# Performance work log

Measured on AMD Instinct MI355X. Metric: run time of the kernel, lower is better.

Reference implementation:

```python
import jax, jax.numpy as jnp
import numpy as np

B, L, DIN, DT, NOUT = 2, 144, 1024, 150, 4


def setup_inputs() -> dict:
    key = jax.random.key(0)
    ks = jax.random.split(key, 7)
    w = lambda k, shape: (jax.random.normal(k, shape, jnp.float32) * 0.02)
    return dict(
        x=jax.random.normal(ks[0], (B, L, DIN), jnp.float32),
        W_sh=w(ks[1], (DIN, DT)), b_sh=jnp.zeros((DT,), jnp.float32),
        W_st=w(ks[2], (DIN, DT)), b_st=jnp.zeros((DT,), jnp.float32),
        W_oh=w(ks[3], (DIN, DT)), b_oh=jnp.zeros((DT,), jnp.float32),
        W_ot=w(ks[4], (DIN, DT)), b_ot=jnp.zeros((DT,), jnp.float32),
        W_tri1=w(ks[5], (NOUT, DT, DT, DT)),
        W_tri2=w(ks[6], (NOUT, DT, DT, DT)),
    )


def _triaffine(x, y, z, W):
    # supar Triaffine convention: out[b,z,x,y,o] = sum_{i,k,j} x[b,x,i] W[o,i,k,j] y[b,y,j] z[b,z,k]
    w = jnp.einsum('bzk,oikj->bzoij', z, W)      # [B,L,o,d,d]
    t = jnp.einsum('bzoij,byj->bzoiy', w, y)     # [B,L,o,d,L]
    return jnp.einsum('bzoiy,bxi->bzxyo', t, x)  # [B,L,L,L,o]


def reference(x, W_sh, b_sh, W_st, b_st, W_oh, b_oh, W_ot, b_ot, W_tri1, W_tri2):
    # MLP projections (dropout is identity at eval time)
    sh = x @ W_sh + b_sh
    st = x @ W_st + b_st
    oh = x @ W_oh + b_oh
    ot = x @ W_ot + b_ot
    n = x.shape[1]
    # torch .triu() on (..., sh, st) keeps entries with sh <= st, zeros the rest
    tri = jnp.arange(n)[:, None] <= jnp.arange(n)[None, :]
    m = tri[None, :, :, None, None]
    # shstoh = Triaffine(st, rel_oh, sh) -> [b, sh, st, oh, o]; triu over (sh, st)
    s1 = _triaffine(st, oh, sh, W_tri1)
    s1 = jnp.where(m, s1, 0.0)
    # shstot = Triaffine(rel_ot, st, sh) -> [b, sh, ot, st, o]; permutes give (b, sh, st, ot, o) with triu over (sh, st)
    s2 = _triaffine(ot, st, sh, W_tri2)
    s2 = jnp.where(m, jnp.transpose(s2, (0, 1, 3, 2, 4)), 0.0)
    return jax.nn.log_softmax(s1, axis=-1), jax.nn.log_softmax(s2, axis=-1)
```

## Files before the change

### kernel.cpp

```cpp
#include <hip/hip_runtime.h>
#include <hip/hip_bf16.h>
#include <math.h>

typedef unsigned short u16;
typedef __attribute__((ext_vector_type(8))) short bf16x8;
typedef __attribute__((ext_vector_type(8))) unsigned short us8;
typedef __attribute__((ext_vector_type(4))) float f32x4;

static __device__ __forceinline__ u16 f2bf(float f) {
  __hip_bfloat16 h = __float2bfloat16(f);
  return *reinterpret_cast<u16*>(&h);
}

__global__ __launch_bounds__(256) void conv_x(const float* __restrict__ x,
                                              u16* __restrict__ xb) {
  int idx = (blockIdx.x * 256 + threadIdx.x) * 4;
  float4 v = *(const float4*)(x + idx);
  ushort4 o;
  o.x = f2bf(v.x); o.y = f2bf(v.y); o.z = f2bf(v.z); o.w = f2bf(v.w);
  *(ushort4*)(xb + idx) = o;
}

__global__ __launch_bounds__(256) void trans_wp(
    const float* __restrict__ W0, const float* __restrict__ W1,
    const float* __restrict__ W2, const float* __restrict__ W3,
    u16* __restrict__ WT4) {
  __shared__ float lds[64 * 151];
  int kt = blockIdx.x, p = blockIdx.y;
  const float* W = (p == 0) ? W0 : (p == 1) ? W1 : (p == 2) ? W2 : W3;
  for (int t = threadIdx.x; t < 64 * 150; t += 256) {
    int k = t / 150, j = t - k * 150;
    lds[k * 151 + j] = W[(size_t)(kt * 64 + k) * 150 + j];
  }
  __syncthreads();
  u16* dst = WT4 + (size_t)p * 160 * 1024 + kt * 64;
  for (int t = threadIdx.x; t < 160 * 64; t += 256) {
    int j = t >> 6, kk = t & 63;
    float v = (j < 150) ? lds[kk * 151 + j] : 0.f;
    dst[(size_t)j * 1024 + kk] = f2bf(v);
  }
}

__global__ __launch_bounds__(256) void transw_kernel(
    const float* __restrict__ W, u16* __restrict__ WtT) {
  __shared__ float lds[150 * 82];
  int oi = blockIdx.x, jh = blockIdx.y;
  const float* src = W + (size_t)oi * 22500 + jh * 80;
  for (int t = threadIdx.x; t < 150 * 40; t += 256) {
    int k = t / 40, c = t - k * 40;
    if (jh * 80 + 2 * c < 150) {
      float2 v = *(const float2*)(src + (size_t)k * 150 + 2 * c);
      *(float2*)&lds[k * 82 + 2 * c] = v;
    }
  }
  __syncthreads();
  u16* dst = WtT + (size_t)oi * 25600 + (size_t)jh * 80 * 160;
  for (int t = threadIdx.x; t < 80 * 20; t += 256) {
    int jl = t / 20, kc = t - jl * 20;
    int j = jh * 80 + jl;
    bool jlive = (j < 150);
    us8 v;
#pragma unroll
    for (int u = 0; u < 8; ++u) {
      int k = kc * 8 + u;
      float f = (jlive && k < 150) ? lds[k * 82 + jl] : 0.f;
      v[u] = f2bf(f);
    }
    *(us8*)(dst + (size_t)jl * 160 + kc * 8) = v;
  }
}

template <int STAGE>
__global__ __launch_bounds__(192) void gemm_ds(
    const u16* __restrict__ A, const u16* __restrict__ B, u16* __restrict__ C,
    int Mvalid, int ZcapW, int ZcapT, const float* __restrict__ bias0,
    const float* __restrict__ bias1, const float* __restrict__ bias2,
    const float* __restrict__ bias3) {
  constexpr int KS = (STAGE == 0) ? 32 : 5;
  constexpr int AS = (STAGE == 0) ? 1024 : 160;
  const u16 *Ab, *Bb;
  u16* Cb = nullptr;
  int cstride = 0;
  int mrow0 = 0;
  if (STAGE == 0) {
    mrow0 = blockIdx.y * 144;
    Ab = A + (size_t)mrow0 * 1024;
    Bb = B + (size_t)blockIdx.x * 80 * 1024;
  } else if (STAGE == 1) {
    int ntile = blockIdx.x, oi = blockIdx.y, b = blockIdx.z;
    int o = oi / 150, i = oi - o * 150;
    Ab = A + (size_t)b * 23040;
    Bb = B + (size_t)oi * 25600 + ntile * 12800;
    Cb = C + (size_t)b * ZcapW + ((size_t)o * 160 + i) * 160 + ntile * 80;
    cstride = 102400;
  } else {
    int ntile = blockIdx.x, f2 = blockIdx.y, b = blockIdx.z;
    Ab = A + (size_t)b * 23040;
    Bb = B + (size_t)b * ZcapW + (size_t)f2 * 25600 + ntile * 12800;
    Cb = C + (size_t)b * ZcapT + (size_t)f2 * 23040 + ntile * 80;
    cstride = 160;
  }
  int tid = threadIdx.x;
  int lane = tid & 63, wave = tid >> 6;
  int l16 = lane & 15, quad = lane >> 4;
  const u16* Ap = Ab + (size_t)(wave * 48 + l16) * AS + quad * 8;
  const u16* Bp = Bb + (size_t)l16 * AS + quad * 8;
  f32x4 acc[3][5];
#pragma unroll
  for (int mi = 0; mi < 3; ++mi)
#pragma unroll
    for (int ni = 0; ni < 5; ++ni) acc[mi][ni] = (f32x4){0.f, 0.f, 0.f, 0.f};

#pragma unroll
  for (int ks = 0; ks < KS; ++ks) {
    bf16x8 af[3], bfr[5];
#pragma unroll
    for (int mi = 0; mi < 3; ++mi)
      af[mi] = *(const bf16x8*)(Ap + (size_t)mi * 16 * AS + ks * 32);
#pragma unroll
    for (int ni = 0; ni < 5; ++ni)
      bfr[ni] = *(const bf16x8*)(Bp + (size_t)ni * 16 * AS + ks * 32);
#pragma unroll
    for (int mi = 0; mi < 3; ++mi)
#pragma unroll
      for (int ni = 0; ni < 5; ++ni)
        acc[mi][ni] = __builtin_amdgcn_mfma_f32_16x16x32_bf16(
            af[mi], bfr[ni], acc[mi][ni], 0, 0, 0);
  }

  if (STAGE == 0) {
    int nbase = blockIdx.x * 80;
#pragma unroll
    for (int ni = 0; ni < 5; ++ni) {
      int n = nbase + ni * 16 + l16;
      int p = n / 160, j = n - p * 160;
      const float* bp =
          (p == 0) ? bias0 : (p == 1) ? bias1 : (p == 2) ? bias2 : bias3;
      bool live = (j < 150);
      float bv = live ? bp[j] : 0.f;
#pragma unroll
      for (int mi = 0; mi < 3; ++mi) {
        int row = mrow0 + wave * 48 + mi * 16 + quad * 4;
#pragma unroll
        for (int r = 0; r < 4; ++r) {
          float v = live ? acc[mi][ni][r] + bv : 0.f;
          C[((size_t)p * 288 + row + r) * 160 + j] = f2bf(v);
        }
      }
    }
  } else {
#pragma unroll
    for (int mi = 0; mi < 3; ++mi) {
      int grow0 = wave * 48 + mi * 16 + quad * 4;
#pragma unroll
      for (int ni = 0; ni < 5; ++ni)
#pragma unroll
        for (int r = 0; r < 4; ++r) {
          int grow = grow0 + r;
          if (grow < Mvalid)
            Cb[(size_t)grow * cstride + ni * 16 + l16] = f2bf(acc[mi][ni][r]);
        }
    }
  }
}

template <int VAR>
__global__ __launch_bounds__(256) void stage3_kernel(
    const u16* __restrict__ tb, const u16* __restrict__ P,
    float* __restrict__ out, int z0, int ZcapT) {
  __shared__ float sf[9216];
  int bx = blockIdx.x;
  int b = bx & 1, xt = (bx >> 1) * 48;
  int yt = blockIdx.y * 48;
  int zl = blockIdx.z;
  int zg = z0 + zl;
  int tid = threadIdx.x;
  const float NL4 = -1.3862943611198906f;
  size_t obase = ((size_t)(b * 144 + zg)) * 82944;
  if (zg > xt + 47) {
    float4 v = make_float4(NL4, NL4, NL4, NL4);
    for (int p = tid; p < 2304; p += 256) {
      int xl = p / 48, yl = p - xl * 48;
      *(float4*)(out + obase + ((size_t)(xt + xl) * 144 + yt + yl) * 4) = v;
    }
    return;
  }
  int pbase = (VAR == 0) ? xt : yt;
  int qbase = (VAR == 0) ? yt : xt;
  int lane = tid & 63, o = tid >> 6, l16 = lane & 15, quad = lane >> 4;
  const u16* Pp = P + (size_t)b * 23040 + (size_t)(pbase + l16) * 160 + quad * 8;
  const u16* Tp = tb + (size_t)b * ZcapT + (size_t)zl * 92160 +
                  (size_t)(o * 144 + qbase + l16) * 160 + quad * 8;
  const u16* Ap = (VAR == 0) ? Pp : Tp;
  const u16* Bp = (VAR == 0) ? Tp : Pp;
  f32x4 acc[3][3];
#pragma unroll
  for (int mi = 0; mi < 3; ++mi)
#pragma unroll
    for (int ni = 0; ni < 3; ++ni) acc[mi][ni] = (f32x4){0.f, 0.f, 0.f, 0.f};

#pragma unroll
  for (int ks = 0; ks < 5; ++ks) {
    bf16x8 af[3], bfr[3];
#pragma unroll
    for (int mi = 0; mi < 3; ++mi)
      af[mi] = *(const bf16x8*)(Ap + (size_t)mi * 16 * 160 + ks * 32);
#pragma unroll
    for (int ni = 0; ni < 3; ++ni)
      bfr[ni] = *(const bf16x8*)(Bp + (size_t)ni * 16 * 160 + ks * 32);
#pragma unroll
    for (int mi = 0; mi < 3; ++mi)
#pragma unroll
      for (int ni = 0; ni < 3; ++ni)
        acc[mi][ni] = __builtin_amdgcn_mfma_f32_16x16x32_bf16(
            af[mi], bfr[ni], acc[mi][ni], 0, 0, 0);
  }

#pragma unroll
  for (int mi = 0; mi < 3; ++mi)
#pragma unroll
    for (int ni = 0; ni < 3; ++ni)
#pragma unroll
      for (int r = 0; r < 4; ++r)
        sf[((mi * 16 + quad * 4 + r) * 48 + ni * 16 + l16) * 4 + o] =
            acc[mi][ni][r];
  __syncthreads();
  for (int p = tid; p < 2304; p += 256) {
    int xl = p / 48, yl = p - xl * 48;
    int xg = xt + xl;
    float4 v;
    if (zg > xg) {
      v = make_float4(NL4, NL4, NL4, NL4);
    } else {
      float c0 = sf[p * 4], c1 = sf[p * 4 + 1];
      float c2 = sf[p * 4 + 2], c3 = sf[p * 4 + 3];
      float mx = fmaxf(fmaxf(c0, c1), fmaxf(c2, c3));
      float l = mx + logf(expf(c0 - mx) + expf(c1 - mx) + expf(c2 - mx) +
                          expf(c3 - mx));
      v = make_float4(c0 - l, c1 - l, c2 - l, c3 - l);
    }
    *(float4*)(out + obase + ((size_t)xg * 144 + yt + yl) * 4) = v;
  }
}

extern "C" void kernel_launch(void* const* d_in, const int* in_sizes, int n_in,
                              void* d_out, int out_size, void* d_ws,
                              size_t ws_size, hipStream_t stream) {
  const float* x = (const float*)d_in[0];
  const float* Wsh = (const float*)d_in[1];
  const float* bsh = (const float*)d_in[2];
  const float* Wst = (const float*)d_in[3];
  const float* bst = (const float*)d_in[4];
  const float* Woh = (const float*)d_in[5];
  const float* boh = (const float*)d_in[6];
  const float* Wot = (const float*)d_in[7];
  const float* bot = (const float*)d_in[8];
  const float* Wt1 = (const float*)d_in[9];
  const float* Wt2 = (const float*)d_in[10];

  u16* ws = (u16*)d_ws;
  u16* xb = ws;
  u16* WT4 = ws + 294912;
  u16* pAll = ws + 950272;
  u16* WtT = ws + 1134592;
  u16* dyn = ws + 16494592;
  size_t ws_u = ws_size / 2;
  long long avail = (long long)ws_u - 16494592LL;
  int Zc = (avail > 0) ? (int)(avail / 389120) : 1;
  if (Zc > 144) Zc = 144;
  if (Zc < 1) Zc = 1;
  int ZcapW = Zc * 102400, ZcapT = Zc * 92160;
  u16* wbuf = dyn;
  u16* tbuf = dyn + (size_t)2 * ZcapW;

  conv_x<<<288, 256, 0, stream>>>(x, xb);
  trans_wp<<<dim3(16, 4), 256, 0, stream>>>(Wsh, Wst, Woh, Wot, WT4);
  gemm_ds<0><<<dim3(8, 2), 192, 0, stream>>>(xb, WT4, pAll, 288, 0, 0, bsh,
                                             bst, boh, bot);

  float* out0 = (float*)d_out;
  float* out1 = out0 + 23887872;

  for (int tri = 0; tri < 2; ++tri) {
    transw_kernel<<<dim3(600, 2), 256, 0, stream>>>(tri ? Wt2 : Wt1, WtT);
    const u16* shsec = pAll;
    const u16* pQ = pAll + (size_t)(tri ? 1 : 2) * 46080;
    const u16* pP = pAll + (size_t)(tri ? 3 : 1) * 46080;
    float* outT = tri ? out1 : out0;
    for (int z0 = 0; z0 < 144; z0 += Zc) {
      int Zcur = (Zc < 144 - z0) ? Zc : (144 - z0);
      gemm_ds<1><<<dim3(2, 600, 2), 192, 0, stream>>>(
          shsec + (size_t)z0 * 160, WtT, wbuf, Zcur, ZcapW, 0, nullptr,
          nullptr, nullptr, nullptr);
      gemm_ds<2><<<dim3(2, Zcur * 4, 2), 192, 0, stream>>>(
          pQ, wbuf, tbuf, 144, ZcapW, ZcapT, nullptr, nullptr, nullptr,
          nullptr);
      dim3 g3(6, 3, Zcur);
      if (tri == 0)
        stage3_kernel<0><<<g3, 256, 0, stream>>>(tbuf, pP, outT, z0, ZcapT);
      else
        stage3_kernel<1><<<g3, 256, 0, stream>>>(tbuf, pP, outT, z0, ZcapT);
    }
  }
}
```

Baseline: 595.9 us.

## Batch both triaffines into single launches with full-size buffers and vectorized stores

```diff
diff --git a/kernel.cpp b/kernel.cpp
--- a/kernel.cpp
+++ b/kernel.cpp
@@ -41,10 +41,12 @@
   }
 }
 
-__global__ __launch_bounds__(256) void transw_kernel(
-    const float* __restrict__ W, u16* __restrict__ WtT) {
+__global__ __launch_bounds__(256) void transw2(const float* __restrict__ Wa,
+                                               const float* __restrict__ Wb,
+                                               u16* __restrict__ WtT) {
   __shared__ float lds[150 * 82];
-  int oi = blockIdx.x, jh = blockIdx.y;
+  int oi = blockIdx.x, jh = blockIdx.y, tri = blockIdx.z;
+  const float* W = tri ? Wb : Wa;
   const float* src = W + (size_t)oi * 22500 + jh * 80;
   for (int t = threadIdx.x; t < 150 * 40; t += 256) {
     int k = t / 40, c = t - k * 40;
@@ -54,7 +56,8 @@
     }
   }
   __syncthreads();
-  u16* dst = WtT + (size_t)oi * 25600 + (size_t)jh * 80 * 160;
+  u16* dst = WtT + (size_t)tri * 15360000 + (size_t)oi * 25600 +
+             (size_t)jh * 80 * 160;
   for (int t = threadIdx.x; t < 80 * 20; t += 256) {
     int jl = t / 20, kc = t - jl * 20;
     int j = jh * 80 + jl;
@@ -71,95 +74,101 @@
 }
 
 template <int STAGE>
-__global__ __launch_bounds__(192) void gemm_ds(
-    const u16* __restrict__ A, const u16* __restrict__ B, u16* __restrict__ C,
-    int Mvalid, int ZcapW, int ZcapT, const float* __restrict__ bias0,
+__global__ __launch_bounds__(192) void gemm_sw(
+    const u16* __restrict__ M0, const u16* __restrict__ N0,
+    u16* __restrict__ C, const float* __restrict__ bias0,
     const float* __restrict__ bias1, const float* __restrict__ bias2,
     const float* __restrict__ bias3) {
   constexpr int KS = (STAGE == 0) ? 32 : 5;
-  constexpr int AS = (STAGE == 0) ? 1024 : 160;
-  const u16 *Ab, *Bb;
+  constexpr int SR = (STAGE == 0) ? 1024 : 160;
+  const u16* Mb;
+  const u16* Nb;
   u16* Cb = nullptr;
-  int cstride = 0;
-  int mrow0 = 0;
   if (STAGE == 0) {
-    mrow0 = blockIdx.y * 144;
-    Ab = A + (size_t)mrow0 * 1024;
-    Bb = B + (size_t)blockIdx.x * 80 * 1024;
+    Mb = M0 + (size_t)blockIdx.x * 80 * 1024;
+    Nb = N0 + (size_t)blockIdx.y * 144 * 1024;
   } else if (STAGE == 1) {
-    int ntile = blockIdx.x, oi = blockIdx.y, b = blockIdx.z;
+    int nt = blockIdx.x, oip = blockIdx.y, b = blockIdx.z;
+    int tri = (oip >= 600) ? 1 : 0;
+    int oi = oip - tri * 600;
     int o = oi / 150, i = oi - o * 150;
-    Ab = A + (size_t)b * 23040;
-    Bb = B + (size_t)oi * 25600 + ntile * 12800;
-    Cb = C + (size_t)b * ZcapW + ((size_t)o * 160 + i) * 160 + ntile * 80;
-    cstride = 102400;
+    Mb = M0 + (size_t)oip * 25600 + nt * 12800;
+    Nb = N0 + (size_t)b * 23040;
+    Cb = C + (size_t)tri * 29491200 + (size_t)b * 14745600 +
+         ((size_t)o * 160 + i) * 160 + nt * 80;
   } else {
-    int ntile = blockIdx.x, f2 = blockIdx.y, b = blockIdx.z;
-    Ab = A + (size_t)b * 23040;
-    Bb = B + (size_t)b * ZcapW + (size_t)f2 * 25600 + ntile * 12800;
-    Cb = C + (size_t)b * ZcapT + (size_t)f2 * 23040 + ntile * 80;
-    cstride = 160;
+    int nt = blockIdx.x, f2p = blockIdx.y, b = blockIdx.z;
+    int tri = (f2p >= 576) ? 1 : 0;
+    int f2 = f2p - tri * 576;
+    int z = f2 >> 2, o = f2 & 3;
+    Mb = M0 + (size_t)tri * 29491200 + (size_t)b * 14745600 +
+         (size_t)z * 102400 + o * 25600 + nt * 12800;
+    Nb = N0 + (size_t)(tri ? 46080 : 92160) + (size_t)b * 23040;
+    Cb = C + (size_t)tri * 26542080 + (size_t)b * 13271040 +
+         (size_t)z * 92160 + o * 23040 + nt * 80;
   }
   int tid = threadIdx.x;
   int lane = tid & 63, wave = tid >> 6;
   int l16 = lane & 15, quad = lane >> 4;
-  const u16* Ap = Ab + (size_t)(wave * 48 + l16) * AS + quad * 8;
-  const u16* Bp = Bb + (size_t)l16 * AS + quad * 8;
-  f32x4 acc[3][5];
-#pragma unroll
-  for (int mi = 0; mi < 3; ++mi)
-#pragma unroll
-    for (int ni = 0; ni < 5; ++ni) acc[mi][ni] = (f32x4){0.f, 0.f, 0.f, 0.f};
+  const u16* Mp = Mb + (size_t)l16 * SR + quad * 8;
+  const u16* Np = Nb + (size_t)(wave * 48 + l16) * SR + quad * 8;
+  f32x4 acc[5][3];
+#pragma unroll
+  for (int mi = 0; mi < 5; ++mi)
+#pragma unroll
+    for (int ni = 0; ni < 3; ++ni) acc[mi][ni] = (f32x4){0.f, 0.f, 0.f, 0.f};
 
 #pragma unroll
   for (int ks = 0; ks < KS; ++ks) {
-    bf16x8 af[3], bfr[5];
-#pragma unroll
-    for (int mi = 0; mi < 3; ++mi)
-      af[mi] = *(const bf16x8*)(Ap + (size_t)mi * 16 * AS + ks * 32);
-#pragma unroll
-    for (int ni = 0; ni < 5; ++ni)
-      bfr[ni] = *(const bf16x8*)(Bp + (size_t)ni * 16 * AS + ks * 32);
-#pragma unroll
-    for (int mi = 0; mi < 3; ++mi)
-#pragma unroll
-      for (int ni = 0; ni < 5; ++ni)
+    bf16x8 mf[5], nf[3];
+#pragma unroll
+    for (int mi = 0; mi < 5; ++mi)
+      mf[mi] = *(const bf16x8*)(Mp + (size_t)mi * 16 * SR + ks * 32);
+#pragma unroll
+    for (int ni = 0; ni < 3; ++ni)
+      nf[ni] = *(const bf16x8*)(Np + (size_t)ni * 16 * SR + ks * 32);
+#pragma unroll
+    for (int mi = 0; mi < 5; ++mi)
+#pragma unroll
+      for (int ni = 0; ni < 3; ++ni)
         acc[mi][ni] = __builtin_amdgcn_mfma_f32_16x16x32_bf16(
-            af[mi], bfr[ni], acc[mi][ni], 0, 0, 0);
+            mf[mi], nf[ni], acc[mi][ni], 0, 0, 0);
   }
 
   if (STAGE == 0) {
-    int nbase = blockIdx.x * 80;
-#pragma unroll
-    for (int ni = 0; ni < 5; ++ni) {
-      int n = nbase + ni * 16 + l16;
-      int p = n / 160, j = n - p * 160;
-      const float* bp =
-          (p == 0) ? bias0 : (p == 1) ? bias1 : (p == 2) ? bias2 : bias3;
-      bool live = (j < 150);
-      float bv = live ? bp[j] : 0.f;
-#pragma unroll
-      for (int mi = 0; mi < 3; ++mi) {
-        int row = mrow0 + wave * 48 + mi * 16 + quad * 4;
-#pragma unroll
-        for (int r = 0; r < 4; ++r) {
-          float v = live ? acc[mi][ni][r] + bv : 0.f;
-          C[((size_t)p * 288 + row + r) * 160 + j] = f2bf(v);
-        }
+    int p = blockIdx.x >> 1;
+    const float* bp =
+        (p == 0) ? bias0 : (p == 1) ? bias1 : (p == 2) ? bias2 : bias3;
+    int jb0 = (blockIdx.x & 1) * 80;
+#pragma unroll
+    for (int mi = 0; mi < 5; ++mi) {
+      int jb = jb0 + mi * 16 + quad * 4;
+#pragma unroll
+      for (int ni = 0; ni < 3; ++ni) {
+        int row = blockIdx.y * 144 + wave * 48 + ni * 16 + l16;
+        ushort4 pk;
+        float v0 = (jb + 0 < 150) ? acc[mi][ni][0] + bp[jb + 0] : 0.f;
+        float v1 = (jb + 1 < 150) ? acc[mi][ni][1] + bp[jb + 1] : 0.f;
+        float v2 = (jb + 2 < 150) ? acc[mi][ni][2] + bp[jb + 2] : 0.f;
+        float v3 = (jb + 3 < 150) ? acc[mi][ni][3] + bp[jb + 3] : 0.f;
+        pk.x = f2bf(v0); pk.y = f2bf(v1); pk.z = f2bf(v2); pk.w = f2bf(v3);
+        *(ushort4*)(C + ((size_t)p * 288 + row) * 160 + jb) = pk;
       }
     }
   } else {
 #pragma unroll
-    for (int mi = 0; mi < 3; ++mi) {
-      int grow0 = wave * 48 + mi * 16 + quad * 4;
-#pragma unroll
-      for (int ni = 0; ni < 5; ++ni)
-#pragma unroll
-        for (int r = 0; r < 4; ++r) {
-          int grow = grow0 + r;
-          if (grow < Mvalid)
-            Cb[(size_t)grow * cstride + ni * 16 + l16] = f2bf(acc[mi][ni][r]);
-        }
+    for (int mi = 0; mi < 5; ++mi) {
+      int mb4 = mi * 16 + quad * 4;
+#pragma unroll
+      for (int ni = 0; ni < 3; ++ni) {
+        int outer = wave * 48 + ni * 16 + l16;
+        ushort4 pk;
+        pk.x = f2bf(acc[mi][ni][0]); pk.y = f2bf(acc[mi][ni][1]);
+        pk.z = f2bf(acc[mi][ni][2]); pk.w = f2bf(acc[mi][ni][3]);
+        size_t off = (STAGE == 1) ? ((size_t)outer * 102400 + mb4)
+                                  : ((size_t)outer * 160 + mb4);
+        *(ushort4*)(Cb + off) = pk;
+      }
     }
   }
 }
@@ -167,13 +176,12 @@
 template <int VAR>
 __global__ __launch_bounds__(256) void stage3_kernel(
     const u16* __restrict__ tb, const u16* __restrict__ P,
-    float* __restrict__ out, int z0, int ZcapT) {
+    float* __restrict__ out, int BT) {
   __shared__ float sf[9216];
   int bx = blockIdx.x;
   int b = bx & 1, xt = (bx >> 1) * 48;
   int yt = blockIdx.y * 48;
-  int zl = blockIdx.z;
-  int zg = z0 + zl;
+  int zg = blockIdx.z;
   int tid = threadIdx.x;
   const float NL4 = -1.3862943611198906f;
   size_t obase = ((size_t)(b * 144 + zg)) * 82944;
@@ -189,7 +197,7 @@
   int qbase = (VAR == 0) ? yt : xt;
   int lane = tid & 63, o = tid >> 6, l16 = lane & 15, quad = lane >> 4;
   const u16* Pp = P + (size_t)b * 23040 + (size_t)(pbase + l16) * 160 + quad * 8;
-  const u16* Tp = tb + (size_t)b * ZcapT + (size_t)zl * 92160 +
+  const u16* Tp = tb + (size_t)b * BT + (size_t)zg * 92160 +
                   (size_t)(o * 144 + qbase + l16) * 160 + quad * 8;
   const u16* Ap = (VAR == 0) ? Pp : Tp;
   const u16* Bp = (VAR == 0) ? Tp : Pp;
@@ -263,43 +271,24 @@
   u16* WT4 = ws + 294912;
   u16* pAll = ws + 950272;
   u16* WtT = ws + 1134592;
-  u16* dyn = ws + 16494592;
-  size_t ws_u = ws_size / 2;
-  long long avail = (long long)ws_u - 16494592LL;
-  int Zc = (avail > 0) ? (int)(avail / 389120) : 1;
-  if (Zc > 144) Zc = 144;
-  if (Zc < 1) Zc = 1;
-  int ZcapW = Zc * 102400, ZcapT = Zc * 92160;
-  u16* wbuf = dyn;
-  u16* tbuf = dyn + (size_t)2 * ZcapW;
+  u16* wbuf = ws + 31854592;
+  u16* tbuf = ws + 90836992;
+  (void)ws_size;
 
   conv_x<<<288, 256, 0, stream>>>(x, xb);
   trans_wp<<<dim3(16, 4), 256, 0, stream>>>(Wsh, Wst, Woh, Wot, WT4);
-  gemm_ds<0><<<dim3(8, 2), 192, 0, stream>>>(xb, WT4, pAll, 288, 0, 0, bsh,
-                                             bst, boh, bot);
+  transw2<<<dim3(600, 2, 2), 256, 0, stream>>>(Wt1, Wt2, WtT);
+  gemm_sw<0><<<dim3(8, 2), 192, 0, stream>>>(WT4, xb, pAll, bsh, bst, boh,
+                                             bot);
+  gemm_sw<1><<<dim3(2, 1200, 2), 192, 0, stream>>>(WtT, pAll, wbuf, nullptr,
+                                                   nullptr, nullptr, nullptr);
+  gemm_sw<2><<<dim3(2, 1152, 2), 192, 0, stream>>>(wbuf, pAll, tbuf, nullptr,
+                                                   nullptr, nullptr, nullptr);
 
   float* out0 = (float*)d_out;
   float* out1 = out0 + 23887872;
-
-  for (int tri = 0; tri < 2; ++tri) {
-    transw_kernel<<<dim3(600, 2), 256, 0, stream>>>(tri ? Wt2 : Wt1, WtT);
-    const u16* shsec = pAll;
-    const u16* pQ = pAll + (size_t)(tri ? 1 : 2) * 46080;
-    const u16* pP = pAll + (size_t)(tri ? 3 : 1) * 46080;
-    float* outT = tri ? out1 : out0;
-    for (int z0 = 0; z0 < 144; z0 += Zc) {
-      int Zcur = (Zc < 144 - z0) ? Zc : (144 - z0);
-      gemm_ds<1><<<dim3(2, 600, 2), 192, 0, stream>>>(
-          shsec + (size_t)z0 * 160, WtT, wbuf, Zcur, ZcapW, 0, nullptr,
-          nullptr, nullptr, nullptr);
-      gemm_ds<2><<<dim3(2, Zcur * 4, 2), 192, 0, stream>>>(
-          pQ, wbuf, tbuf, 144, ZcapW, ZcapT, nullptr, nullptr, nullptr,
-          nullptr);
-      dim3 g3(6, 3, Zcur);
-      if (tri == 0)
-        stage3_kernel<0><<<g3, 256, 0, stream>>>(tbuf, pP, outT, z0, ZcapT);
-      else
-        stage3_kernel<1><<<g3, 256, 0, stream>>>(tbuf, pP, outT, z0, ZcapT);
-    }
-  }
-}
+  stage3_kernel<0><<<dim3(6, 3, 144), 256, 0, stream>>>(
+      tbuf, pAll + 46080, out0, 13271040);
+  stage3_kernel<1><<<dim3(6, 3, 144), 256, 0, stream>>>(
+      tbuf + 26542080, pAll + 138240, out1, 13271040);
+}
```

Measured after the change: 621.5 us. +4.3%, slower.
